# Optimization experiments

Measured on AMD Instinct MI355X. Metric: run time of the kernel, lower is better.

## Reference

```python
import jax, jax.numpy as jnp
import numpy as np

N_NODES = 50000
N_EDGES = 800000
D_IN = 128
D_HID = 128
N_CLASSES = 16
N_GRAPHS = 256


def _gcn_norm(edge_index, num_nodes):
    # PyG GCNConv default: add self-loops, symmetric normalization.
    loops = jnp.arange(num_nodes, dtype=edge_index.dtype)
    src = jnp.concatenate([edge_index[0], loops])
    dst = jnp.concatenate([edge_index[1], loops])
    deg = jax.ops.segment_sum(jnp.ones_like(src, dtype=jnp.float32), dst,
                              num_segments=num_nodes)
    dinv = jnp.where(deg > 0, jax.lax.rsqrt(deg), 0.0)
    norm = dinv[src] * dinv[dst]  # [E + N]
    return src, dst, norm


def _gcn_conv(x, src, dst, norm, W, b, num_nodes):
    h = x @ W                                  # [N, d_out] dense GEMM
    msg = h[src] * norm[:, None]               # gather + scale [E+N, d_out]
    agg = jax.ops.segment_sum(msg, dst, num_segments=num_nodes)
    return agg + b


def setup_inputs() -> dict:
    key = jax.random.key(0)
    ks = jax.random.split(key, 10)
    x = jax.random.normal(ks[0], (N_NODES, D_IN), dtype=jnp.float32)
    edge_index = jax.random.randint(ks[1], (2, N_EDGES), 0, N_NODES, dtype=jnp.int64)
    batch = jnp.sort(jax.random.randint(ks[2], (N_NODES,), 0, N_GRAPHS, dtype=jnp.int64))
    s1 = 1.0 / np.sqrt(D_IN)
    s2 = 1.0 / np.sqrt(D_HID)
    W1 = jax.random.uniform(ks[3], (D_IN, D_HID), jnp.float32, -s1, s1)
    b1 = jnp.zeros((D_HID,), jnp.float32)
    W2 = jax.random.uniform(ks[4], (D_HID, D_HID), jnp.float32, -s2, s2)
    b2 = jnp.zeros((D_HID,), jnp.float32)
    Wc = jax.random.uniform(ks[5], (D_HID, N_CLASSES), jnp.float32, -s2, s2)
    bc = jnp.zeros((N_CLASSES,), jnp.float32)
    return {"x": x, "edge_index": edge_index, "batch": batch,
            "W1": W1, "b1": b1, "W2": W2, "b2": b2, "Wc": Wc, "bc": bc}


def reference(x, edge_index, batch, W1, b1, W2, b2, Wc, bc):
    src, dst, norm = _gcn_norm(edge_index, N_NODES)
    h = _gcn_conv(x, src, dst, norm, W1, b1, N_NODES)
    h = jax.nn.relu(h)  # dropout is identity in eval mode
    h = _gcn_conv(h, src, dst, norm, W2, b2, N_NODES)
    # global mean pool over graph ids
    sums = jax.ops.segment_sum(h, batch, num_segments=N_GRAPHS)
    cnts = jax.ops.segment_sum(jnp.ones((N_NODES,), jnp.float32), batch,
                               num_segments=N_GRAPHS)
    pooled = sums / jnp.maximum(cnts, 1.0)[:, None]  # [G, D_HID]
    return pooled @ Wc + bc  # [G, N_CLASSES]
```

## Files before the change

### kernel.cpp

```cpp
#include <hip/hip_runtime.h>

#define N_NODES 50000
#define N_EDGES 800000
#define D 128
#define N_GRAPHS 256
#define N_CLASSES 16
#define NB_SCAN ((N_NODES + 255) / 256)

typedef unsigned short ushort_t;
typedef unsigned int uint_t;
typedef unsigned char uchar_t;
typedef __attribute__((ext_vector_type(8))) short bf16x8;
typedef __attribute__((ext_vector_type(4))) float f32x4;

__device__ __forceinline__ float bf2f(uint_t u) {
  return __uint_as_float(u << 16);
}
__device__ __forceinline__ uint_t f2bf(float f) {
  uint_t x = __float_as_uint(f);
  return (x + 0x7fffu + ((x >> 16) & 1u)) >> 16;
}

__global__ void k_pre(const int* __restrict__ ei, int* __restrict__ deg,
                      uchar_t* __restrict__ rank) {
  int e = blockIdx.x * blockDim.x + threadIdx.x;
  if (e < N_EDGES) {
    int d = ei[N_EDGES + e];
    int r = atomicAdd(&deg[d], 1);
    rank[e] = (uchar_t)r;
  }
}

__global__ __launch_bounds__(256) void k_wprep(const float* __restrict__ W1,
                                               const float* __restrict__ W2,
                                               uint4* __restrict__ W1f,
                                               uint4* __restrict__ W2f) {
  int slot = blockIdx.x * 256 + threadIdx.x;
  const float* W = (slot < 2048) ? W1 : W2;
  uint4* Wf = (slot < 2048) ? W1f : W2f;
  int sl = slot & 2047;
  int lane = sl & 63;
  int s = (sl >> 6) & 3;
  int n = sl >> 8;
  int col = n * 16 + (lane & 15);
  int k0 = s * 32 + (lane >> 4) * 8;
  uint4 o;
  o.x = f2bf(W[(size_t)(k0 + 0) * D + col]) | (f2bf(W[(size_t)(k0 + 1) * D + col]) << 16);
  o.y = f2bf(W[(size_t)(k0 + 2) * D + col]) | (f2bf(W[(size_t)(k0 + 3) * D + col]) << 16);
  o.z = f2bf(W[(size_t)(k0 + 4) * D + col]) | (f2bf(W[(size_t)(k0 + 5) * D + col]) << 16);
  o.w = f2bf(W[(size_t)(k0 + 6) * D + col]) | (f2bf(W[(size_t)(k0 + 7) * D + col]) << 16);
  Wf[sl] = o;
}

__global__ __launch_bounds__(256) void k_bsum(const int* __restrict__ deg,
                                              float* __restrict__ dinv,
                                              int* __restrict__ bsum) {
  int t = threadIdx.x;
  int i = blockIdx.x * 256 + t;
  int d = 0;
  if (i < N_NODES) {
    d = deg[i];
    dinv[i] = rsqrtf((float)(d + 1));
  }
#pragma unroll
  for (int o = 1; o < 64; o <<= 1) d += __shfl_xor(d, o);
  __shared__ int ws[4];
  if ((t & 63) == 0) ws[t >> 6] = d;
  __syncthreads();
  if (t == 0) bsum[blockIdx.x] = ws[0] + ws[1] + ws[2] + ws[3];
}

__global__ __launch_bounds__(256) void k_spart(const int* __restrict__ bsum,
                                               const int* __restrict__ batch,
                                               int* __restrict__ bpre,
                                               int* __restrict__ offs,
                                               float* __restrict__ rcnts) {
  int t = threadIdx.x;
  int lane = t & 63, wid = t >> 6;
  int d = (t < NB_SCAN) ? bsum[t] : 0;
  int v = d;
#pragma unroll
  for (int o = 1; o < 64; o <<= 1) {
    int u = __shfl_up(v, o);
    if (lane >= o) v += u;
  }
  __shared__ int ws[4];
  __shared__ int bound[256];
  if (lane == 63) ws[wid] = v;
  {
    int g = t;
    int lo = 0, hi = N_NODES;
    while (lo < hi) {
      int m = (lo + hi) >> 1;
      if (batch[m] < g) lo = m + 1; else hi = m;
    }
    bound[g] = lo;
  }
  __syncthreads();
  int add = 0;
  for (int w = 0; w < wid; ++w) add += ws[w];
  int excl = v - d + add;
  if (t < NB_SCAN) bpre[t] = excl;
  if (t == NB_SCAN - 1) offs[N_NODES] = excl + d;
  int cnt = ((t == 255) ? N_NODES : bound[t + 1]) - bound[t];
  rcnts[t] = 1.0f / (float)max(cnt, 1);
}

__global__ __launch_bounds__(256) void k_fill(const int* __restrict__ deg,
                                              const int* __restrict__ bpre,
                                              int* __restrict__ offs) {
  int t = threadIdx.x;
  int i = blockIdx.x * 256 + t;
  int d = (i < N_NODES) ? deg[i] : 0;
  int lane = t & 63, wid = t >> 6;
  int v = d;
#pragma unroll
  for (int o = 1; o < 64; o <<= 1) {
    int u = __shfl_up(v, o);
    if (lane >= o) v += u;
  }
  __shared__ int ws[4];
  if (lane == 63) ws[wid] = v;
  __syncthreads();
  int add = bpre[blockIdx.x];
  for (int w = 0; w < wid; ++w) add += ws[w];
  int excl = v - d + add;
  if (i < N_NODES) offs[i] = excl;
}

__global__ void k_csr(const int* __restrict__ ei, const float* __restrict__ dinv,
                      const int* __restrict__ offs, const uchar_t* __restrict__ rank,
                      int2* __restrict__ csr) {
  int e = blockIdx.x * blockDim.x + threadIdx.x;
  if (e >= N_EDGES) return;
  int s = ei[e];
  int d = ei[N_EDGES + e];
  int pos = offs[d] + (int)rank[e];
  float w = dinv[s] * dinv[d];
  csr[pos] = make_int2(s, __float_as_int(w));
}

template <typename TIN>
__global__ __launch_bounds__(256) void k_gemm_mfma(const TIN* __restrict__ A,
                                                   const uint4* __restrict__ Wf,
                                                   ushort_t* __restrict__ Out) {
  int t = threadIdx.x;
  int wv = t >> 6, lane = t & 63;
  int row16 = lane & 15, chunk = lane >> 4;
  int row0 = blockIdx.x * 64 + wv * 16;
  int arow = row0 + row16;
  if (arow >= N_NODES) arow = 0;
  bf16x8 afrag[4];
  if constexpr (sizeof(TIN) == 4) {
    const float* Ar = A + (size_t)arow * D + chunk * 8;
#pragma unroll
    for (int s = 0; s < 4; ++s) {
      float4 lo = *(const float4*)(Ar + s * 32);
      float4 hi = *(const float4*)(Ar + s * 32 + 4);
      uint4 u;
      u.x = f2bf(lo.x) | (f2bf(lo.y) << 16);
      u.y = f2bf(lo.z) | (f2bf(lo.w) << 16);
      u.z = f2bf(hi.x) | (f2bf(hi.y) << 16);
      u.w = f2bf(hi.z) | (f2bf(hi.w) << 16);
      afrag[s] = *(bf16x8*)&u;
    }
  } else {
    const ushort_t* Ar = A + (size_t)arow * D + chunk * 8;
#pragma unroll
    for (int s = 0; s < 4; ++s) afrag[s] = *(const bf16x8*)(Ar + s * 32);
  }
  f32x4 acc[8];
#pragma unroll
  for (int n = 0; n < 8; ++n) acc[n] = (f32x4){0.f, 0.f, 0.f, 0.f};
  const bf16x8* Wb = (const bf16x8*)Wf;
#pragma unroll
  for (int n = 0; n < 8; ++n) {
#pragma unroll
    for (int s = 0; s < 4; ++s) {
      bf16x8 b = Wb[(n * 4 + s) * 64 + lane];
      acc[n] = __builtin_amdgcn_mfma_f32_16x16x32_bf16(afrag[s], b, acc[n], 0, 0, 0);
    }
  }
  int crow0 = row0 + chunk * 4;
#pragma unroll
  for (int n = 0; n < 8; ++n) {
#pragma unroll
    for (int j = 0; j < 4; ++j) {
      int r = crow0 + j;
      if (r < N_NODES)
        Out[(size_t)r * D + n * 16 + row16] = (ushort_t)f2bf(acc[n][j]);
    }
  }
}

__global__ __launch_bounds__(256) void k_agg_relu(const ushort_t* __restrict__ h,
                                                  const int2* __restrict__ csr,
                                                  const int* __restrict__ offs,
                                                  const float* __restrict__ dinv,
                                                  const float* __restrict__ bias,
                                                  ushort_t* __restrict__ obf) {
  int wv = threadIdx.x >> 6;
  int lane = threadIdx.x & 63;
  int node = blockIdx.x * 4 + wv;
  int grp = lane >> 4;
  int gl = lane & 15;
  int d0 = gl * 8;
  int beg = offs[node], end = offs[node + 1];
  float acc[8] = {0.f, 0.f, 0.f, 0.f, 0.f, 0.f, 0.f, 0.f};
  for (int base = beg + grp; base < end; base += 4) {
    int2 e = csr[base];
    float w = __int_as_float(e.y);
    uint4 v = *(const uint4*)(h + (size_t)e.x * D + d0);
    acc[0] = fmaf(w, bf2f(v.x & 0xffffu), acc[0]);
    acc[1] = fmaf(w, bf2f(v.x >> 16), acc[1]);
    acc[2] = fmaf(w, bf2f(v.y & 0xffffu), acc[2]);
    acc[3] = fmaf(w, bf2f(v.y >> 16), acc[3]);
    acc[4] = fmaf(w, bf2f(v.z & 0xffffu), acc[4]);
    acc[5] = fmaf(w, bf2f(v.z >> 16), acc[5]);
    acc[6] = fmaf(w, bf2f(v.w & 0xffffu), acc[6]);
    acc[7] = fmaf(w, bf2f(v.w >> 16), acc[7]);
  }
#pragma unroll
  for (int m = 16; m <= 32; m <<= 1) {
#pragma unroll
    for (int i = 0; i < 8; ++i) acc[i] += __shfl_xor(acc[i], m);
  }
  if (grp == 0) {
    float dn = dinv[node];
    float wsl = dn * dn;
    uint4 v = *(const uint4*)(h + (size_t)node * D + d0);
    acc[0] = fmaf(wsl, bf2f(v.x & 0xffffu), acc[0]);
    acc[1] = fmaf(wsl, bf2f(v.x >> 16), acc[1]);
    acc[2] = fmaf(wsl, bf2f(v.y & 0xffffu), acc[2]);
    acc[3] = fmaf(wsl, bf2f(v.y >> 16), acc[3]);
    acc[4] = fmaf(wsl, bf2f(v.z & 0xffffu), acc[4]);
    acc[5] = fmaf(wsl, bf2f(v.z >> 16), acc[5]);
    acc[6] = fmaf(wsl, bf2f(v.w & 0xffffu), acc[6]);
    acc[7] = fmaf(wsl, bf2f(v.w >> 16), acc[7]);
    float4 blo = *(const float4*)(bias + d0);
    float4 bhi = *(const float4*)(bias + d0 + 4);
    acc[0] += blo.x; acc[1] += blo.y; acc[2] += blo.z; acc[3] += blo.w;
    acc[4] += bhi.x; acc[5] += bhi.y; acc[6] += bhi.z; acc[7] += bhi.w;
#pragma unroll
    for (int i = 0; i < 8; ++i) acc[i] = fmaxf(acc[i], 0.f);
    uint4 o;
    o.x = f2bf(acc[0]) | (f2bf(acc[1]) << 16);
    o.y = f2bf(acc[2]) | (f2bf(acc[3]) << 16);
    o.z = f2bf(acc[4]) | (f2bf(acc[5]) << 16);
    o.w = f2bf(acc[6]) | (f2bf(acc[7]) << 16);
    *(uint4*)(obf + (size_t)node * D + d0) = o;
  }
}

__global__ __launch_bounds__(256) void k_agg_pool(const ushort_t* __restrict__ h,
                                                   const int2* __restrict__ csr,
                                                   const int* __restrict__ offs,
                                                   const float* __restrict__ dinv,
                                                   const int* __restrict__ batch,
                                                   const float* __restrict__ rcnts,
                                                   float* __restrict__ sums) {
  __shared__ float pool[128];
  int t = threadIdx.x;
  int wv = t >> 6, lane = t & 63;
  int grp = lane >> 4, gl = lane & 15;
  int d0 = gl * 8;
  int node0 = blockIdx.x * 16;
  int g0 = batch[node0];
  if (t < 128) pool[t] = 0.f;
  __syncthreads();
  float pacc[8] = {0.f, 0.f, 0.f, 0.f, 0.f, 0.f, 0.f, 0.f};
  for (int i = 0; i < 4; ++i) {
    int node = node0 + wv * 4 + i;
    int beg = offs[node], end = offs[node + 1];
    float acc[8] = {0.f, 0.f, 0.f, 0.f, 0.f, 0.f, 0.f, 0.f};
    for (int base = beg + grp; base < end; base += 4) {
      int2 e = csr[base];
      float w = __int_as_float(e.y);
      uint4 v = *(const uint4*)(h + (size_t)e.x * D + d0);
      acc[0] = fmaf(w, bf2f(v.x & 0xffffu), acc[0]);
      acc[1] = fmaf(w, bf2f(v.x >> 16), acc[1]);
      acc[2] = fmaf(w, bf2f(v.y & 0xffffu), acc[2]);
      acc[3] = fmaf(w, bf2f(v.y >> 16), acc[3]);
      acc[4] = fmaf(w, bf2f(v.z & 0xffffu), acc[4]);
      acc[5] = fmaf(w, bf2f(v.z >> 16), acc[5]);
      acc[6] = fmaf(w, bf2f(v.w & 0xffffu), acc[6]);
      acc[7] = fmaf(w, bf2f(v.w >> 16), acc[7]);
    }
#pragma unroll
    for (int m = 16; m <= 32; m <<= 1) {
#pragma unroll
      for (int k = 0; k < 8; ++k) acc[k] += __shfl_xor(acc[k], m);
    }
    if (grp == 0) {
      float dn = dinv[node];
      float wsl = dn * dn;
      uint4 v = *(const uint4*)(h + (size_t)node * D + d0);
      acc[0] = fmaf(wsl, bf2f(v.x & 0xffffu), acc[0]);
      acc[1] = fmaf(wsl, bf2f(v.x >> 16), acc[1]);
      acc[2] = fmaf(wsl, bf2f(v.y & 0xffffu), acc[2]);
      acc[3] = fmaf(wsl, bf2f(v.y >> 16), acc[3]);
      acc[4] = fmaf(wsl, bf2f(v.z & 0xffffu), acc[4]);
      acc[5] = fmaf(wsl, bf2f(v.z >> 16), acc[5]);
      acc[6] = fmaf(wsl, bf2f(v.w & 0xffffu), acc[6]);
      acc[7] = fmaf(wsl, bf2f(v.w >> 16), acc[7]);
      int g = batch[node];
      float rc = rcnts[g];
      if (g == g0) {
#pragma unroll
        for (int k = 0; k < 8; ++k) pacc[k] = fmaf(acc[k], rc, pacc[k]);
      } else {
#pragma unroll
        for (int k = 0; k < 8; ++k)
          atomicAdd(&sums[(size_t)g * D + d0 + k], acc[k] * rc);
      }
    }
  }
  if (grp == 0) {
#pragma unroll
    for (int k = 0; k < 8; ++k) atomicAdd(&pool[d0 + k], pacc[k]);
  }
  __syncthreads();
  if (t < 128) atomicAdd(&sums[(size_t)g0 * D + t], pool[t]);
}

__global__ __launch_bounds__(128) void k_final(const float* __restrict__ sums,
                                               const float* __restrict__ b2,
                                               const float* __restrict__ Wc,
                                               const float* __restrict__ bc,
                                               float* __restrict__ out) {
  __shared__ float p[128];
  int g = blockIdx.x;
  int t = threadIdx.x;
  p[t] = sums[g * D + t] + b2[t];
  __syncthreads();
  if (t < N_CLASSES) {
    float acc = bc[t];
    for (int k = 0; k < D; ++k) acc = fmaf(p[k], Wc[k * N_CLASSES + t], acc);
    out[g * N_CLASSES + t] = acc;
  }
}

extern "C" void kernel_launch(void* const* d_in, const int* in_sizes, int n_in,
                              void* d_out, int out_size, void* d_ws, size_t ws_size,
                              hipStream_t stream) {
  const float* x = (const float*)d_in[0];
  const int* ei = (const int*)d_in[1];
  const int* batch = (const int*)d_in[2];
  const float* W1 = (const float*)d_in[3];
  const float* b1 = (const float*)d_in[4];
  const float* W2 = (const float*)d_in[5];
  const float* b2 = (const float*)d_in[6];
  const float* Wc = (const float*)d_in[7];
  const float* bc = (const float*)d_in[8];
  float* out = (float*)d_out;

  char* ws = (char*)d_ws;
  size_t off = 0;
  auto alloc = [&](size_t bytes) -> void* {
    void* p = (void*)(ws + off);
    off += (bytes + 255) & ~(size_t)255;
    return p;
  };
  int* deg = (int*)alloc((size_t)N_NODES * 4);
  float* sums = (float*)alloc((size_t)N_GRAPHS * D * 4);
  size_t zero_bytes = off;
  int* offs = (int*)alloc((size_t)(N_NODES + 1) * 4);
  float* dinv = (float*)alloc((size_t)N_NODES * 4);
  float* rcnts = (float*)alloc((size_t)N_GRAPHS * 4);
  int* bsum = (int*)alloc((size_t)NB_SCAN * 4);
  int* bpre = (int*)alloc((size_t)NB_SCAN * 4);
  uchar_t* rank = (uchar_t*)alloc((size_t)N_EDGES);
  uint4* W1f = (uint4*)alloc((size_t)2048 * 16);
  uint4* W2f = (uint4*)alloc((size_t)2048 * 16);
  int2* csr = (int2*)alloc((size_t)N_EDGES * 8);
  ushort_t* hbuf = (ushort_t*)alloc((size_t)N_NODES * D * 2);
  ushort_t* x2 = (ushort_t*)alloc((size_t)N_NODES * D * 2);

  hipMemsetAsync(ws, 0, zero_bytes, stream);

  k_pre<<<(N_EDGES + 255) / 256, 256, 0, stream>>>(ei, deg, rank);
  k_wprep<<<16, 256, 0, stream>>>(W1, W2, W1f, W2f);
  k_bsum<<<NB_SCAN, 256, 0, stream>>>(deg, dinv, bsum);
  k_spart<<<1, 256, 0, stream>>>(bsum, batch, bpre, offs, rcnts);
  k_fill<<<NB_SCAN, 256, 0, stream>>>(deg, bpre, offs);
  k_csr<<<(N_EDGES + 255) / 256, 256, 0, stream>>>(ei, dinv, offs, rank, csr);

  k_gemm_mfma<float><<<(N_NODES + 63) / 64, 256, 0, stream>>>(x, W1f, hbuf);
  k_agg_relu<<<N_NODES / 4, 256, 0, stream>>>(hbuf, csr, offs, dinv, b1, x2);
  k_gemm_mfma<ushort_t><<<(N_NODES + 63) / 64, 256, 0, stream>>>(x2, W2f, hbuf);
  k_agg_pool<<<N_NODES / 16, 256, 0, stream>>>(hbuf, csr, offs, dinv, batch, rcnts, sums);

  k_final<<<N_GRAPHS, 128, 0, stream>>>(sums, b2, Wc, bc, out);
}
```

Baseline: 262.6 us.

## Assign one node per 16-lane group and unroll edge gathers by four

The aggregation kernels now give each 16-thread group a whole node instead of splitting one node's edges across four groups of a wave. This removes the cross-group shuffle reductions and the idle-lane epilogue. The edge loop reads CSR entries as 16-byte pairs and issues four independent row gathers per iteration to raise memory-level parallelism. In exchange, lanes in a wave now handle nodes of different degree and can diverge, and the pool kernel does more shared-memory atomics per node.

```diff
diff --git a/kernel.cpp b/kernel.cpp
--- a/kernel.cpp
+++ b/kernel.cpp
@@ -19,6 +19,16 @@
 __device__ __forceinline__ uint_t f2bf(float f) {
   uint_t x = __float_as_uint(f);
   return (x + 0x7fffu + ((x >> 16) & 1u)) >> 16;
+}
+__device__ __forceinline__ void fma8(float* acc, float w, uint4 v) {
+  acc[0] = fmaf(w, bf2f(v.x & 0xffffu), acc[0]);
+  acc[1] = fmaf(w, bf2f(v.x >> 16), acc[1]);
+  acc[2] = fmaf(w, bf2f(v.y & 0xffffu), acc[2]);
+  acc[3] = fmaf(w, bf2f(v.y >> 16), acc[3]);
+  acc[4] = fmaf(w, bf2f(v.z & 0xffffu), acc[4]);
+  acc[5] = fmaf(w, bf2f(v.z >> 16), acc[5]);
+  acc[6] = fmaf(w, bf2f(v.w & 0xffffu), acc[6]);
+  acc[7] = fmaf(w, bf2f(v.w >> 16), acc[7]);
 }
 
 __global__ void k_pre(const int* __restrict__ ei, int* __restrict__ deg,
@@ -193,63 +203,72 @@
   }
 }
 
+__device__ __forceinline__ void agg_edges(const ushort_t* __restrict__ h,
+                                          const int2* __restrict__ csr,
+                                          int beg, int end, int d0, float* acc) {
+  int base = beg;
+  if ((base & 1) && base < end) {
+    int2 e = csr[base];
+    uint4 v = *(const uint4*)(h + (size_t)e.x * D + d0);
+    fma8(acc, __int_as_float(e.y), v);
+    ++base;
+  }
+  for (; base + 4 <= end; base += 4) {
+    int4 e01 = *(const int4*)(csr + base);
+    int4 e23 = *(const int4*)(csr + base + 2);
+    uint4 v0 = *(const uint4*)(h + (size_t)e01.x * D + d0);
+    uint4 v1 = *(const uint4*)(h + (size_t)e01.z * D + d0);
+    uint4 v2 = *(const uint4*)(h + (size_t)e23.x * D + d0);
+    uint4 v3 = *(const uint4*)(h + (size_t)e23.z * D + d0);
+    fma8(acc, __int_as_float(e01.y), v0);
+    fma8(acc, __int_as_float(e01.w), v1);
+    fma8(acc, __int_as_float(e23.y), v2);
+    fma8(acc, __int_as_float(e23.w), v3);
+  }
+  if (base + 2 <= end) {
+    int4 e01 = *(const int4*)(csr + base);
+    uint4 v0 = *(const uint4*)(h + (size_t)e01.x * D + d0);
+    uint4 v1 = *(const uint4*)(h + (size_t)e01.z * D + d0);
+    fma8(acc, __int_as_float(e01.y), v0);
+    fma8(acc, __int_as_float(e01.w), v1);
+    base += 2;
+  }
+  if (base < end) {
+    int2 e = csr[base];
+    uint4 v = *(const uint4*)(h + (size_t)e.x * D + d0);
+    fma8(acc, __int_as_float(e.y), v);
+  }
+}
+
 __global__ __launch_bounds__(256) void k_agg_relu(const ushort_t* __restrict__ h,
                                                   const int2* __restrict__ csr,
                                                   const int* __restrict__ offs,
                                                   const float* __restrict__ dinv,
                                                   const float* __restrict__ bias,
                                                   ushort_t* __restrict__ obf) {
-  int wv = threadIdx.x >> 6;
-  int lane = threadIdx.x & 63;
-  int node = blockIdx.x * 4 + wv;
-  int grp = lane >> 4;
-  int gl = lane & 15;
+  int t = threadIdx.x;
+  int grp = t >> 4;
+  int gl = t & 15;
   int d0 = gl * 8;
+  int node = blockIdx.x * 16 + grp;
   int beg = offs[node], end = offs[node + 1];
   float acc[8] = {0.f, 0.f, 0.f, 0.f, 0.f, 0.f, 0.f, 0.f};
-  for (int base = beg + grp; base < end; base += 4) {
-    int2 e = csr[base];
-    float w = __int_as_float(e.y);
-    uint4 v = *(const uint4*)(h + (size_t)e.x * D + d0);
-    acc[0] = fmaf(w, bf2f(v.x & 0xffffu), acc[0]);
-    acc[1] = fmaf(w, bf2f(v.x >> 16), acc[1]);
-    acc[2] = fmaf(w, bf2f(v.y & 0xffffu), acc[2]);
-    acc[3] = fmaf(w, bf2f(v.y >> 16), acc[3]);
-    acc[4] = fmaf(w, bf2f(v.z & 0xffffu), acc[4]);
-    acc[5] = fmaf(w, bf2f(v.z >> 16), acc[5]);
-    acc[6] = fmaf(w, bf2f(v.w & 0xffffu), acc[6]);
-    acc[7] = fmaf(w, bf2f(v.w >> 16), acc[7]);
-  }
-#pragma unroll
-  for (int m = 16; m <= 32; m <<= 1) {
-#pragma unroll
-    for (int i = 0; i < 8; ++i) acc[i] += __shfl_xor(acc[i], m);
-  }
-  if (grp == 0) {
-    float dn = dinv[node];
-    float wsl = dn * dn;
-    uint4 v = *(const uint4*)(h + (size_t)node * D + d0);
-    acc[0] = fmaf(wsl, bf2f(v.x & 0xffffu), acc[0]);
-    acc[1] = fmaf(wsl, bf2f(v.x >> 16), acc[1]);
-    acc[2] = fmaf(wsl, bf2f(v.y & 0xffffu), acc[2]);
-    acc[3] = fmaf(wsl, bf2f(v.y >> 16), acc[3]);
-    acc[4] = fmaf(wsl, bf2f(v.z & 0xffffu), acc[4]);
-    acc[5] = fmaf(wsl, bf2f(v.z >> 16), acc[5]);
-    acc[6] = fmaf(wsl, bf2f(v.w & 0xffffu), acc[6]);
-    acc[7] = fmaf(wsl, bf2f(v.w >> 16), acc[7]);
-    float4 blo = *(const float4*)(bias + d0);
-    float4 bhi = *(const float4*)(bias + d0 + 4);
-    acc[0] += blo.x; acc[1] += blo.y; acc[2] += blo.z; acc[3] += blo.w;
-    acc[4] += bhi.x; acc[5] += bhi.y; acc[6] += bhi.z; acc[7] += bhi.w;
-#pragma unroll
-    for (int i = 0; i < 8; ++i) acc[i] = fmaxf(acc[i], 0.f);
-    uint4 o;
-    o.x = f2bf(acc[0]) | (f2bf(acc[1]) << 16);
-    o.y = f2bf(acc[2]) | (f2bf(acc[3]) << 16);
-    o.z = f2bf(acc[4]) | (f2bf(acc[5]) << 16);
-    o.w = f2bf(acc[6]) | (f2bf(acc[7]) << 16);
-    *(uint4*)(obf + (size_t)node * D + d0) = o;
-  }
+  agg_edges(h, csr, beg, end, d0, acc);
+  float dn = dinv[node];
+  uint4 v = *(const uint4*)(h + (size_t)node * D + d0);
+  fma8(acc, dn * dn, v);
+  float4 blo = *(const float4*)(bias + d0);
+  float4 bhi = *(const float4*)(bias + d0 + 4);
+  acc[0] += blo.x; acc[1] += blo.y; acc[2] += blo.z; acc[3] += blo.w;
+  acc[4] += bhi.x; acc[5] += bhi.y; acc[6] += bhi.z; acc[7] += bhi.w;
+#pragma unroll
+  for (int i = 0; i < 8; ++i) acc[i] = fmaxf(acc[i], 0.f);
+  uint4 o;
+  o.x = f2bf(acc[0]) | (f2bf(acc[1]) << 16);
+  o.y = f2bf(acc[2]) | (f2bf(acc[3]) << 16);
+  o.z = f2bf(acc[4]) | (f2bf(acc[5]) << 16);
+  o.w = f2bf(acc[6]) | (f2bf(acc[7]) << 16);
+  *(uint4*)(obf + (size_t)node * D + d0) = o;
 }
 
 __global__ __launch_bounds__(256) void k_agg_pool(const ushort_t* __restrict__ h,
@@ -261,63 +280,29 @@
                                                    float* __restrict__ sums) {
   __shared__ float pool[128];
   int t = threadIdx.x;
-  int wv = t >> 6, lane = t & 63;
-  int grp = lane >> 4, gl = lane & 15;
+  int grp = t >> 4;
+  int gl = t & 15;
   int d0 = gl * 8;
   int node0 = blockIdx.x * 16;
+  int node = node0 + grp;
   int g0 = batch[node0];
   if (t < 128) pool[t] = 0.f;
   __syncthreads();
-  float pacc[8] = {0.f, 0.f, 0.f, 0.f, 0.f, 0.f, 0.f, 0.f};
-  for (int i = 0; i < 4; ++i) {
-    int node = node0 + wv * 4 + i;
-    int beg = offs[node], end = offs[node + 1];
-    float acc[8] = {0.f, 0.f, 0.f, 0.f, 0.f, 0.f, 0.f, 0.f};
-    for (int base = beg + grp; base < end; base += 4) {
-      int2 e = csr[base];
-      float w = __int_as_float(e.y);
-      uint4 v = *(const uint4*)(h + (size_t)e.x * D + d0);
-      acc[0] = fmaf(w, bf2f(v.x & 0xffffu), acc[0]);
-      acc[1] = fmaf(w, bf2f(v.x >> 16), acc[1]);
-      acc[2] = fmaf(w, bf2f(v.y & 0xffffu), acc[2]);
-      acc[3] = fmaf(w, bf2f(v.y >> 16), acc[3]);
-      acc[4] = fmaf(w, bf2f(v.z & 0xffffu), acc[4]);
-      acc[5] = fmaf(w, bf2f(v.z >> 16), acc[5]);
-      acc[6] = fmaf(w, bf2f(v.w & 0xffffu), acc[6]);
-      acc[7] = fmaf(w, bf2f(v.w >> 16), acc[7]);
-    }
-#pragma unroll
-    for (int m = 16; m <= 32; m <<= 1) {
-#pragma unroll
-      for (int k = 0; k < 8; ++k) acc[k] += __shfl_xor(acc[k], m);
-    }
-    if (grp == 0) {
-      float dn = dinv[node];
-      float wsl = dn * dn;
-      uint4 v = *(const uint4*)(h + (size_t)node * D + d0);
-      acc[0] = fmaf(wsl, bf2f(v.x & 0xffffu), acc[0]);
-      acc[1] = fmaf(wsl, bf2f(v.x >> 16), acc[1]);
-      acc[2] = fmaf(wsl, bf2f(v.y & 0xffffu), acc[2]);
-      acc[3] = fmaf(wsl, bf2f(v.y >> 16), acc[3]);
-      acc[4] = fmaf(wsl, bf2f(v.z & 0xffffu), acc[4]);
-      acc[5] = fmaf(wsl, bf2f(v.z >> 16), acc[5]);
-      acc[6] = fmaf(wsl, bf2f(v.w & 0xffffu), acc[6]);
-      acc[7] = fmaf(wsl, bf2f(v.w >> 16), acc[7]);
-      int g = batch[node];
-      float rc = rcnts[g];
-      if (g == g0) {
-#pragma unroll
-        for (int k = 0; k < 8; ++k) pacc[k] = fmaf(acc[k], rc, pacc[k]);
-      } else {
-#pragma unroll
-        for (int k = 0; k < 8; ++k)
-          atomicAdd(&sums[(size_t)g * D + d0 + k], acc[k] * rc);
-      }
-    }
-  }
-  if (grp == 0) {
-#pragma unroll
-    for (int k = 0; k < 8; ++k) atomicAdd(&pool[d0 + k], pacc[k]);
+  int beg = offs[node], end = offs[node + 1];
+  float acc[8] = {0.f, 0.f, 0.f, 0.f, 0.f, 0.f, 0.f, 0.f};
+  agg_edges(h, csr, beg, end, d0, acc);
+  float dn = dinv[node];
+  uint4 v = *(const uint4*)(h + (size_t)node * D + d0);
+  fma8(acc, dn * dn, v);
+  int g = batch[node];
+  float rc = rcnts[g];
+  if (g == g0) {
+#pragma unroll
+    for (int k = 0; k < 8; ++k) atomicAdd(&pool[d0 + k], acc[k] * rc);
+  } else {
+#pragma unroll
+    for (int k = 0; k < 8; ++k)
+      atomicAdd(&sums[(size_t)g * D + d0 + k], acc[k] * rc);
   }
   __syncthreads();
   if (t < 128) atomicAdd(&sums[(size_t)g0 * D + t], pool[t]);
@@ -386,7 +371,7 @@
   k_csr<<<(N_EDGES + 255) / 256, 256, 0, stream>>>(ei, dinv, offs, rank, csr);
 
   k_gemm_mfma<float><<<(N_NODES + 63) / 64, 256, 0, stream>>>(x, W1f, hbuf);
-  k_agg_relu<<<N_NODES / 4, 256, 0, stream>>>(hbuf, csr, offs, dinv, b1, x2);
+  k_agg_relu<<<N_NODES / 16, 256, 0, stream>>>(hbuf, csr, offs, dinv, b1, x2);
   k_gemm_mfma<ushort_t><<<(N_NODES + 63) / 64, 256, 0, stream>>>(x2, W2f, hbuf);
   k_agg_pool<<<N_NODES / 16, 256, 0, stream>>>(hbuf, csr, offs, dinv, batch, rcnts, sums);
 
```

Result: no change. 265.9 us (+1.3%).

## Fold GCN normalization into GEMM epilogue and use padded index-only CSR

Applied to the files above, without the earlier changes.

Factors the symmetric normalization so the GEMM epilogue scales each row by dinv[src], and aggregation multiplies by dinv[dst] once per node. The CSR can then store only 4-byte source indices instead of (index, weight) pairs. Each node's segment is padded to a multiple of 4, so one 16-byte vector load fetches four indices and four gathers can be issued at once. This halves CSR bytes and removes per-edge multiplies. In exchange the segments are padded, the lanes take a less even share of edges, and the rounding changes slightly because dinv is applied before the bf16 conversion.

```diff
diff --git a/kernel.cpp b/kernel.cpp
--- a/kernel.cpp
+++ b/kernel.cpp
@@ -12,6 +12,7 @@
 typedef unsigned char uchar_t;
 typedef __attribute__((ext_vector_type(8))) short bf16x8;
 typedef __attribute__((ext_vector_type(4))) float f32x4;
+typedef __attribute__((ext_vector_type(4))) int i32x4;
 
 __device__ __forceinline__ float bf2f(uint_t u) {
   return __uint_as_float(u << 16);
@@ -19,6 +20,16 @@
 __device__ __forceinline__ uint_t f2bf(float f) {
   uint_t x = __float_as_uint(f);
   return (x + 0x7fffu + ((x >> 16) & 1u)) >> 16;
+}
+__device__ __forceinline__ void add8(float* acc, uint4 v) {
+  acc[0] += bf2f(v.x & 0xffffu);
+  acc[1] += bf2f(v.x >> 16);
+  acc[2] += bf2f(v.y & 0xffffu);
+  acc[3] += bf2f(v.y >> 16);
+  acc[4] += bf2f(v.z & 0xffffu);
+  acc[5] += bf2f(v.z >> 16);
+  acc[6] += bf2f(v.w & 0xffffu);
+  acc[7] += bf2f(v.w >> 16);
 }
 
 __global__ void k_pre(const int* __restrict__ ei, int* __restrict__ deg,
@@ -57,15 +68,16 @@
                                               int* __restrict__ bsum) {
   int t = threadIdx.x;
   int i = blockIdx.x * 256 + t;
-  int d = 0;
+  int pd = 0;
   if (i < N_NODES) {
-    d = deg[i];
+    int d = deg[i];
     dinv[i] = rsqrtf((float)(d + 1));
-  }
-#pragma unroll
-  for (int o = 1; o < 64; o <<= 1) d += __shfl_xor(d, o);
+    pd = (d + 3) & ~3;
+  }
+#pragma unroll
+  for (int o = 1; o < 64; o <<= 1) pd += __shfl_xor(pd, o);
   __shared__ int ws[4];
-  if ((t & 63) == 0) ws[t >> 6] = d;
+  if ((t & 63) == 0) ws[t >> 6] = pd;
   __syncthreads();
   if (t == 0) bsum[blockIdx.x] = ws[0] + ws[1] + ws[2] + ws[3];
 }
@@ -73,7 +85,6 @@
 __global__ __launch_bounds__(256) void k_spart(const int* __restrict__ bsum,
                                                const int* __restrict__ batch,
                                                int* __restrict__ bpre,
-                                               int* __restrict__ offs,
                                                float* __restrict__ rcnts) {
   int t = threadIdx.x;
   int lane = t & 63, wid = t >> 6;
@@ -99,9 +110,7 @@
   __syncthreads();
   int add = 0;
   for (int w = 0; w < wid; ++w) add += ws[w];
-  int excl = v - d + add;
-  if (t < NB_SCAN) bpre[t] = excl;
-  if (t == NB_SCAN - 1) offs[N_NODES] = excl + d;
+  if (t < NB_SCAN) bpre[t] = v - d + add;
   int cnt = ((t == 255) ? N_NODES : bound[t + 1]) - bound[t];
   rcnts[t] = 1.0f / (float)max(cnt, 1);
 }
@@ -111,9 +120,9 @@
                                               int* __restrict__ offs) {
   int t = threadIdx.x;
   int i = blockIdx.x * 256 + t;
-  int d = (i < N_NODES) ? deg[i] : 0;
+  int pd = (i < N_NODES) ? ((deg[i] + 3) & ~3) : 0;
   int lane = t & 63, wid = t >> 6;
-  int v = d;
+  int v = pd;
 #pragma unroll
   for (int o = 1; o < 64; o <<= 1) {
     int u = __shfl_up(v, o);
@@ -124,25 +133,22 @@
   __syncthreads();
   int add = bpre[blockIdx.x];
   for (int w = 0; w < wid; ++w) add += ws[w];
-  int excl = v - d + add;
-  if (i < N_NODES) offs[i] = excl;
-}
-
-__global__ void k_csr(const int* __restrict__ ei, const float* __restrict__ dinv,
-                      const int* __restrict__ offs, const uchar_t* __restrict__ rank,
-                      int2* __restrict__ csr) {
+  if (i < N_NODES) offs[i] = v - pd + add;
+}
+
+__global__ void k_csr(const int* __restrict__ ei, const int* __restrict__ offs,
+                      const uchar_t* __restrict__ rank, int* __restrict__ csr) {
   int e = blockIdx.x * blockDim.x + threadIdx.x;
   if (e >= N_EDGES) return;
   int s = ei[e];
   int d = ei[N_EDGES + e];
-  int pos = offs[d] + (int)rank[e];
-  float w = dinv[s] * dinv[d];
-  csr[pos] = make_int2(s, __float_as_int(w));
+  __builtin_nontemporal_store(s, csr + offs[d] + (int)rank[e]);
 }
 
 template <typename TIN>
 __global__ __launch_bounds__(256) void k_gemm_mfma(const TIN* __restrict__ A,
                                                    const uint4* __restrict__ Wf,
+                                                   const float* __restrict__ dinv,
                                                    ushort_t* __restrict__ Out) {
   int t = threadIdx.x;
   int wv = t >> 6, lane = t & 63;
@@ -182,65 +188,75 @@
     }
   }
   int crow0 = row0 + chunk * 4;
+  float dv[4];
+#pragma unroll
+  for (int j = 0; j < 4; ++j)
+    dv[j] = (crow0 + j < N_NODES) ? dinv[crow0 + j] : 0.f;
 #pragma unroll
   for (int n = 0; n < 8; ++n) {
 #pragma unroll
     for (int j = 0; j < 4; ++j) {
       int r = crow0 + j;
       if (r < N_NODES)
-        Out[(size_t)r * D + n * 16 + row16] = (ushort_t)f2bf(acc[n][j]);
-    }
+        Out[(size_t)r * D + n * 16 + row16] = (ushort_t)f2bf(acc[n][j] * dv[j]);
+    }
+  }
+}
+
+__device__ __forceinline__ void agg_core(const ushort_t* __restrict__ h,
+                                         const int* __restrict__ csr,
+                                         int beg, int end, int grp, int d0,
+                                         float* acc) {
+  for (int wb = beg; wb < end; wb += 16) {
+    int i0 = wb + grp * 4;
+    i32x4 s4 = __builtin_nontemporal_load((const i32x4*)(csr + i0));
+    bool b0 = i0 < end, b1 = i0 + 1 < end, b2 = i0 + 2 < end, b3 = i0 + 3 < end;
+    uint4 v0, v1, v2, v3;
+    if (b0) v0 = *(const uint4*)(h + (size_t)s4.x * D + d0);
+    if (b1) v1 = *(const uint4*)(h + (size_t)s4.y * D + d0);
+    if (b2) v2 = *(const uint4*)(h + (size_t)s4.z * D + d0);
+    if (b3) v3 = *(const uint4*)(h + (size_t)s4.w * D + d0);
+    if (b0) add8(acc, v0);
+    if (b1) add8(acc, v1);
+    if (b2) add8(acc, v2);
+    if (b3) add8(acc, v3);
   }
 }
 
 __global__ __launch_bounds__(256) void k_agg_relu(const ushort_t* __restrict__ h,
-                                                  const int2* __restrict__ csr,
+                                                  const int* __restrict__ csr,
                                                   const int* __restrict__ offs,
+                                                  const int* __restrict__ deg,
                                                   const float* __restrict__ dinv,
                                                   const float* __restrict__ bias,
                                                   ushort_t* __restrict__ obf) {
-  int wv = threadIdx.x >> 6;
-  int lane = threadIdx.x & 63;
+  int t = threadIdx.x;
+  int wv = t >> 6, lane = t & 63;
+  int grp = lane >> 4, gl = lane & 15;
+  int d0 = gl * 8;
   int node = blockIdx.x * 4 + wv;
-  int grp = lane >> 4;
-  int gl = lane & 15;
-  int d0 = gl * 8;
-  int beg = offs[node], end = offs[node + 1];
+  int beg = offs[node], end = beg + deg[node];
   float acc[8] = {0.f, 0.f, 0.f, 0.f, 0.f, 0.f, 0.f, 0.f};
-  for (int base = beg + grp; base < end; base += 4) {
-    int2 e = csr[base];
-    float w = __int_as_float(e.y);
-    uint4 v = *(const uint4*)(h + (size_t)e.x * D + d0);
-    acc[0] = fmaf(w, bf2f(v.x & 0xffffu), acc[0]);
-    acc[1] = fmaf(w, bf2f(v.x >> 16), acc[1]);
-    acc[2] = fmaf(w, bf2f(v.y & 0xffffu), acc[2]);
-    acc[3] = fmaf(w, bf2f(v.y >> 16), acc[3]);
-    acc[4] = fmaf(w, bf2f(v.z & 0xffffu), acc[4]);
-    acc[5] = fmaf(w, bf2f(v.z >> 16), acc[5]);
-    acc[6] = fmaf(w, bf2f(v.w & 0xffffu), acc[6]);
-    acc[7] = fmaf(w, bf2f(v.w >> 16), acc[7]);
-  }
+  agg_core(h, csr, beg, end, grp, d0, acc);
 #pragma unroll
   for (int m = 16; m <= 32; m <<= 1) {
 #pragma unroll
     for (int i = 0; i < 8; ++i) acc[i] += __shfl_xor(acc[i], m);
   }
   if (grp == 0) {
-    float dn = dinv[node];
-    float wsl = dn * dn;
     uint4 v = *(const uint4*)(h + (size_t)node * D + d0);
-    acc[0] = fmaf(wsl, bf2f(v.x & 0xffffu), acc[0]);
-    acc[1] = fmaf(wsl, bf2f(v.x >> 16), acc[1]);
-    acc[2] = fmaf(wsl, bf2f(v.y & 0xffffu), acc[2]);
-    acc[3] = fmaf(wsl, bf2f(v.y >> 16), acc[3]);
-    acc[4] = fmaf(wsl, bf2f(v.z & 0xffffu), acc[4]);
-    acc[5] = fmaf(wsl, bf2f(v.z >> 16), acc[5]);
-    acc[6] = fmaf(wsl, bf2f(v.w & 0xffffu), acc[6]);
-    acc[7] = fmaf(wsl, bf2f(v.w >> 16), acc[7]);
+    add8(acc, v);
+    float sc = dinv[node];
     float4 blo = *(const float4*)(bias + d0);
     float4 bhi = *(const float4*)(bias + d0 + 4);
-    acc[0] += blo.x; acc[1] += blo.y; acc[2] += blo.z; acc[3] += blo.w;
-    acc[4] += bhi.x; acc[5] += bhi.y; acc[6] += bhi.z; acc[7] += bhi.w;
+    acc[0] = fmaf(acc[0], sc, blo.x);
+    acc[1] = fmaf(acc[1], sc, blo.y);
+    acc[2] = fmaf(acc[2], sc, blo.z);
+    acc[3] = fmaf(acc[3], sc, blo.w);
+    acc[4] = fmaf(acc[4], sc, bhi.x);
+    acc[5] = fmaf(acc[5], sc, bhi.y);
+    acc[6] = fmaf(acc[6], sc, bhi.z);
+    acc[7] = fmaf(acc[7], sc, bhi.w);
 #pragma unroll
     for (int i = 0; i < 8; ++i) acc[i] = fmaxf(acc[i], 0.f);
     uint4 o;
@@ -253,8 +269,9 @@
 }
 
 __global__ __launch_bounds__(256) void k_agg_pool(const ushort_t* __restrict__ h,
-                                                   const int2* __restrict__ csr,
+                                                   const int* __restrict__ csr,
                                                    const int* __restrict__ offs,
+                                                   const int* __restrict__ deg,
                                                    const float* __restrict__ dinv,
                                                    const int* __restrict__ batch,
                                                    const float* __restrict__ rcnts,
@@ -271,47 +288,26 @@
   float pacc[8] = {0.f, 0.f, 0.f, 0.f, 0.f, 0.f, 0.f, 0.f};
   for (int i = 0; i < 4; ++i) {
     int node = node0 + wv * 4 + i;
-    int beg = offs[node], end = offs[node + 1];
+    int beg = offs[node], end = beg + deg[node];
     float acc[8] = {0.f, 0.f, 0.f, 0.f, 0.f, 0.f, 0.f, 0.f};
-    for (int base = beg + grp; base < end; base += 4) {
-      int2 e = csr[base];
-      float w = __int_as_float(e.y);
-      uint4 v = *(const uint4*)(h + (size_t)e.x * D + d0);
-      acc[0] = fmaf(w, bf2f(v.x & 0xffffu), acc[0]);
-      acc[1] = fmaf(w, bf2f(v.x >> 16), acc[1]);
-      acc[2] = fmaf(w, bf2f(v.y & 0xffffu), acc[2]);
-      acc[3] = fmaf(w, bf2f(v.y >> 16), acc[3]);
-      acc[4] = fmaf(w, bf2f(v.z & 0xffffu), acc[4]);
-      acc[5] = fmaf(w, bf2f(v.z >> 16), acc[5]);
-      acc[6] = fmaf(w, bf2f(v.w & 0xffffu), acc[6]);
-      acc[7] = fmaf(w, bf2f(v.w >> 16), acc[7]);
-    }
+    agg_core(h, csr, beg, end, grp, d0, acc);
 #pragma unroll
     for (int m = 16; m <= 32; m <<= 1) {
 #pragma unroll
       for (int k = 0; k < 8; ++k) acc[k] += __shfl_xor(acc[k], m);
     }
     if (grp == 0) {
-      float dn = dinv[node];
-      float wsl = dn * dn;
       uint4 v = *(const uint4*)(h + (size_t)node * D + d0);
-      acc[0] = fmaf(wsl, bf2f(v.x & 0xffffu), acc[0]);
-      acc[1] = fmaf(wsl, bf2f(v.x >> 16), acc[1]);
-      acc[2] = fmaf(wsl, bf2f(v.y & 0xffffu), acc[2]);
-      acc[3] = fmaf(wsl, bf2f(v.y >> 16), acc[3]);
-      acc[4] = fmaf(wsl, bf2f(v.z & 0xffffu), acc[4]);
-      acc[5] = fmaf(wsl, bf2f(v.z >> 16), acc[5]);
-      acc[6] = fmaf(wsl, bf2f(v.w & 0xffffu), acc[6]);
-      acc[7] = fmaf(wsl, bf2f(v.w >> 16), acc[7]);
+      add8(acc, v);
       int g = batch[node];
-      float rc = rcnts[g];
+      float sc = dinv[node] * rcnts[g];
       if (g == g0) {
 #pragma unroll
-        for (int k = 0; k < 8; ++k) pacc[k] = fmaf(acc[k], rc, pacc[k]);
+        for (int k = 0; k < 8; ++k) pacc[k] = fmaf(acc[k], sc, pacc[k]);
       } else {
 #pragma unroll
         for (int k = 0; k < 8; ++k)
-          atomicAdd(&sums[(size_t)g * D + d0 + k], acc[k] * rc);
+          atomicAdd(&sums[(size_t)g * D + d0 + k], acc[k] * sc);
       }
     }
   }
@@ -364,7 +360,7 @@
   int* deg = (int*)alloc((size_t)N_NODES * 4);
   float* sums = (float*)alloc((size_t)N_GRAPHS * D * 4);
   size_t zero_bytes = off;
-  int* offs = (int*)alloc((size_t)(N_NODES + 1) * 4);
+  int* offs = (int*)alloc((size_t)N_NODES * 4);
   float* dinv = (float*)alloc((size_t)N_NODES * 4);
   float* rcnts = (float*)alloc((size_t)N_GRAPHS * 4);
   int* bsum = (int*)alloc((size_t)NB_SCAN * 4);
@@ -372,7 +368,7 @@
   uchar_t* rank = (uchar_t*)alloc((size_t)N_EDGES);
   uint4* W1f = (uint4*)alloc((size_t)2048 * 16);
   uint4* W2f = (uint4*)alloc((size_t)2048 * 16);
-  int2* csr = (int2*)alloc((size_t)N_EDGES * 8);
+  int* csr = (int*)alloc(((size_t)N_EDGES + 3 * N_NODES + 16) * 4);
   ushort_t* hbuf = (ushort_t*)alloc((size_t)N_NODES * D * 2);
   ushort_t* x2 = (ushort_t*)alloc((size_t)N_NODES * D * 2);
 
@@ -381,14 +377,14 @@
   k_pre<<<(N_EDGES + 255) / 256, 256, 0, stream>>>(ei, deg, rank);
   k_wprep<<<16, 256, 0, stream>>>(W1, W2, W1f, W2f);
   k_bsum<<<NB_SCAN, 256, 0, stream>>>(deg, dinv, bsum);
-  k_spart<<<1, 256, 0, stream>>>(bsum, batch, bpre, offs, rcnts);
+  k_spart<<<1, 256, 0, stream>>>(bsum, batch, bpre, rcnts);
   k_fill<<<NB_SCAN, 256, 0, stream>>>(deg, bpre, offs);
-  k_csr<<<(N_EDGES + 255) / 256, 256, 0, stream>>>(ei, dinv, offs, rank, csr);
-
-  k_gemm_mfma<float><<<(N_NODES + 63) / 64, 256, 0, stream>>>(x, W1f, hbuf);
-  k_agg_relu<<<N_NODES / 4, 256, 0, stream>>>(hbuf, csr, offs, dinv, b1, x2);
-  k_gemm_mfma<ushort_t><<<(N_NODES + 63) / 64, 256, 0, stream>>>(x2, W2f, hbuf);
-  k_agg_pool<<<N_NODES / 16, 256, 0, stream>>>(hbuf, csr, offs, dinv, batch, rcnts, sums);
+  k_csr<<<(N_EDGES + 255) / 256, 256, 0, stream>>>(ei, offs, rank, csr);
+
+  k_gemm_mfma<float><<<(N_NODES + 63) / 64, 256, 0, stream>>>(x, W1f, dinv, hbuf);
+  k_agg_relu<<<N_NODES / 4, 256, 0, stream>>>(hbuf, csr, offs, deg, dinv, b1, x2);
+  k_gemm_mfma<ushort_t><<<(N_NODES + 63) / 64, 256, 0, stream>>>(x2, W2f, dinv, hbuf);
+  k_agg_pool<<<N_NODES / 16, 256, 0, stream>>>(hbuf, csr, offs, deg, dinv, batch, rcnts, sums);
 
   k_final<<<N_GRAPHS, 128, 0, stream>>>(sums, b2, Wc, bc, out);
 }
```

After: 270.6 us. 1.03x slower.
